# Kernel optimization log

Measured on AMD Instinct MI355X. Metric: run time of the kernel, lower is better.

## Reference

```python
import jax, jax.numpy as jnp
import numpy as np

KSIZE = 3  # module init kwarg


def setup_inputs() -> dict:
    key = jax.random.key(0)
    k1, k2, k3 = jax.random.split(key, 3)
    shape = (16, 3, 512, 512)  # [B, C, H, W]
    return {
        "sr": jax.random.normal(k1, shape, jnp.float32),
        "sr_ema": jax.random.normal(k2, shape, jnp.float32),
        "hr": jax.random.normal(k3, shape, jnp.float32),
    }


def _local_var(res, ksize):
    """Unbiased variance over a ksize x ksize sliding window with reflect pad.

    Matches torch: reflect-pad then unfold + var(unbiased=True). Implemented as a
    box-filter over sum and sum-of-squares (no ksize^2-larger unfold tensor).
    res: [B, 1, H, W] -> [B, 1, H, W]
    """
    pad = (ksize - 1) // 2
    rp = jnp.pad(res, ((0, 0), (0, 0), (pad, pad), (pad, pad)), mode="reflect")
    n = ksize * ksize
    win = (1, 1, ksize, ksize)
    strides = (1, 1, 1, 1)
    zero = jnp.zeros((), rp.dtype)
    s = jax.lax.reduce_window(rp, zero, jax.lax.add, win, strides, "VALID")
    sq = jax.lax.reduce_window(rp * rp, zero, jax.lax.add, win, strides, "VALID")
    # unbiased: (sum(x^2) - sum(x)^2/n) / (n-1)
    return (sq - s * s / n) / (n - 1)


def reference(sr, sr_ema, hr):
    # per-pixel channel-summed residuals, [B, 1, H, W]
    residual_ema = jnp.sum(jnp.abs(hr - sr_ema), axis=1, keepdims=True) / 255.0
    residual_sr = jnp.sum(jnp.abs(hr - sr), axis=1, keepdims=True) / 255.0

    r_det = jax.lax.stop_gradient(residual_sr)  # .clone().detach() in torch

    # patch-level weight: unbiased var over (C=1, H, W) per sample, ** (1/5)
    n_patch = r_det.shape[1] * r_det.shape[2] * r_det.shape[3]
    mean = jnp.mean(r_det, axis=(-1, -2, -3), keepdims=True)
    patch_var = jnp.sum((r_det - mean) ** 2, axis=(-1, -2, -3), keepdims=True) / (n_patch - 1)
    patch_w = patch_var ** 0.2  # [B,1,1,1]

    pixel_w = _local_var(r_det, KSIZE)  # [B,1,H,W]

    overall_w = patch_w * pixel_w
    overall_w = jnp.where(residual_sr < residual_ema, jnp.zeros((), overall_w.dtype), overall_w)

    # L1 loss (mean reduction) between weighted sr and weighted hr
    return jnp.mean(jnp.abs(overall_w * sr - overall_w * hr))
```

## Files before the change

kernel.cpp:

```cpp
#include <hip/hip_runtime.h>
#include <math.h>


#define BB 16
#define HH 512
#define WW 512
#define HW (HH * WW)
#define CHW (3 * HW)
#define STRIPS 128
#define NBLOCKS (BB * STRIPS)
#define NREGIONS NBLOCKS
#define REG_PER_B STRIPS

__device__ __forceinline__ int reflect_h(int gh) {
  gh = gh < 0 ? -gh : gh;
  return gh >= HH ? 2 * HH - 2 - gh : gh;
}

__global__ __launch_bounds__(256, 8) void wl1_main(
    const float* __restrict__ sr, const float* __restrict__ srema,
    const float* __restrict__ hr, float* __restrict__ p_sum,
    float* __restrict__ p_sum2, float* __restrict__ p_loss) {
  __shared__ float rt[6][WW];
  __shared__ float ft[4][WW];
  const int tid = threadIdx.x;
  const int bid = blockIdx.x;
  const int b = bid >> 7;
  const int h0 = (bid & 127) << 2;
  const float* __restrict__ srb = sr + (size_t)b * CHW;
  const float* __restrict__ hrb = hr + (size_t)b * CHW;
  const float* __restrict__ emb = srema + (size_t)b * CHW;

#pragma unroll
  for (int it = 0; it < 3; ++it) {
    const int item = it * 256 + tid;
    const int row = item >> 7;
    const int g = item & 127;
    const int gh = reflect_h(h0 - 1 + row);
    const float* hp = hrb + gh * WW + 4 * g;
    const float* sp = srb + gh * WW + 4 * g;
    float4 h0v = *(const float4*)hp;
    float4 h1v = *(const float4*)(hp + HW);
    float4 h2v = *(const float4*)(hp + 2 * HW);
    float4 s0v = *(const float4*)sp;
    float4 s1v = *(const float4*)(sp + HW);
    float4 s2v = *(const float4*)(sp + 2 * HW);
    float4 r4;
    r4.x = (fabsf(h0v.x - s0v.x) + fabsf(h1v.x - s1v.x) + fabsf(h2v.x - s2v.x)) / 255.0f;
    r4.y = (fabsf(h0v.y - s0v.y) + fabsf(h1v.y - s1v.y) + fabsf(h2v.y - s2v.y)) / 255.0f;
    r4.z = (fabsf(h0v.z - s0v.z) + fabsf(h1v.z - s1v.z) + fabsf(h2v.z - s2v.z)) / 255.0f;
    r4.w = (fabsf(h0v.w - s0v.w) + fabsf(h1v.w - s1v.w) + fabsf(h2v.w - s2v.w)) / 255.0f;
    *(float4*)&rt[row][4 * g] = r4;
    if (row >= 1 && row <= 4) {
      const float* ep = emb + gh * WW + 4 * g;
      float4 e0v = *(const float4*)ep;
      float4 e1v = *(const float4*)(ep + HW);
      float4 e2v = *(const float4*)(ep + 2 * HW);
      float4 e4, f4;
      e4.x = (fabsf(h0v.x - e0v.x) + fabsf(h1v.x - e1v.x) + fabsf(h2v.x - e2v.x)) / 255.0f;
      e4.y = (fabsf(h0v.y - e0v.y) + fabsf(h1v.y - e1v.y) + fabsf(h2v.y - e2v.y)) / 255.0f;
      e4.z = (fabsf(h0v.z - e0v.z) + fabsf(h1v.z - e1v.z) + fabsf(h2v.z - e2v.z)) / 255.0f;
      e4.w = (fabsf(h0v.w - e0v.w) + fabsf(h1v.w - e1v.w) + fabsf(h2v.w - e2v.w)) / 255.0f;
      f4.x = (r4.x >= e4.x) ? 255.0f * r4.x : 0.0f;
      f4.y = (r4.y >= e4.y) ? 255.0f * r4.y : 0.0f;
      f4.z = (r4.z >= e4.z) ? 255.0f * r4.z : 0.0f;
      f4.w = (r4.w >= e4.w) ? 255.0f * r4.w : 0.0f;
      *(float4*)&ft[row - 1][4 * g] = f4;
    }
  }
  __syncthreads();

  const int g = tid & 127;
  const int r0 = tid >> 7;
  const int li = (g == 0) ? 1 : 4 * g - 1;
  const int ri = (g == 127) ? 510 : 4 * g + 4;
  float v1 = 0.f, v2 = 0.f, v3 = 0.f;
#pragma unroll
  for (int k = 0; k < 2; ++k) {
    const int orow = r0 + 2 * k;
    float cs[6] = {0, 0, 0, 0, 0, 0}, cq[6] = {0, 0, 0, 0, 0, 0};
    float center[4];
#pragma unroll
    for (int dr = 0; dr < 3; ++dr) {
      const int row = orow + dr;
      float4 c4 = *(const float4*)&rt[row][4 * g];
      float lv = rt[row][li];
      float rv = rt[row][ri];
      float v[6] = {lv, c4.x, c4.y, c4.z, c4.w, rv};
#pragma unroll
      for (int j = 0; j < 6; ++j) {
        cs[j] += v[j];
        cq[j] += v[j] * v[j];
      }
      if (dr == 1) { center[0] = c4.x; center[1] = c4.y; center[2] = c4.z; center[3] = c4.w; }
    }
    float4 f4 = *(const float4*)&ft[orow][4 * g];
    const float fv[4] = {f4.x, f4.y, f4.z, f4.w};
#pragma unroll
    for (int c = 0; c < 4; ++c) {
      float s = cs[c] + cs[c + 1] + cs[c + 2];
      float q = cq[c] + cq[c + 1] + cq[c + 2];
      float pvar = (q - s * s / 9.0f) / 8.0f;
      float rc = center[c];
      v1 += rc;
      v2 += rc * rc;
      v3 += pvar * fv[c];
    }
  }

#pragma unroll
  for (int off = 32; off > 0; off >>= 1) {
    v1 += __shfl_down(v1, off, 64);
    v2 += __shfl_down(v2, off, 64);
    v3 += __shfl_down(v3, off, 64);
  }
  __syncthreads();
  const int wave = tid >> 6, lane = tid & 63;
  if (lane == 0) {
    rt[0][wave] = v1;
    rt[0][8 + wave] = v2;
    rt[0][16 + wave] = v3;
  }
  __syncthreads();
  if (tid == 0) {
    p_sum[bid] = rt[0][0] + rt[0][1] + rt[0][2] + rt[0][3];
    p_sum2[bid] = rt[0][8] + rt[0][9] + rt[0][10] + rt[0][11];
    p_loss[bid] = rt[0][16] + rt[0][17] + rt[0][18] + rt[0][19];
  }
}

__global__ __launch_bounds__(1024) void wl1_reduce(
    const float* __restrict__ p_sum, const float* __restrict__ p_sum2,
    const float* __restrict__ p_loss, float* __restrict__ out) {
  const int tid = threadIdx.x;
  const int b = tid >> 6, k = tid & 63;
  double s = 0.0, s2 = 0.0, sl = 0.0;
#pragma unroll
  for (int j = 0; j < REG_PER_B; j += 64) {
    int i = b * REG_PER_B + j + k;
    s += (double)p_sum[i];
    s2 += (double)p_sum2[i];
    sl += (double)p_loss[i];
  }
#pragma unroll
  for (int off = 32; off > 0; off >>= 1) {
    s += __shfl_down(s, off, 64);
    s2 += __shfl_down(s2, off, 64);
    sl += __shfl_down(sl, off, 64);
  }
  __shared__ double acc[BB];
  if (k == 0) {
    const double n = (double)HW;
    double var = (s2 - s * s / n) / (n - 1.0);
    acc[b] = pow(var, 0.2) * sl;
  }
  __syncthreads();
  if (tid == 0) {
    double tot = 0.0;
#pragma unroll
    for (int j = 0; j < BB; ++j) tot += acc[j];
    out[0] = (float)(tot / (double)((size_t)BB * CHW));
  }
}

extern "C" void kernel_launch(void* const* d_in, const int* in_sizes, int n_in,
                              void* d_out, int out_size, void* d_ws,
                              size_t ws_size, hipStream_t stream) {
  const float* sr = (const float*)d_in[0];
  const float* srema = (const float*)d_in[1];
  const float* hr = (const float*)d_in[2];
  float* out = (float*)d_out;

  float* p_sum = (float*)d_ws;
  float* p_sum2 = p_sum + NREGIONS;
  float* p_loss = p_sum2 + NREGIONS;

  wl1_main<<<NBLOCKS, 256, 0, stream>>>(sr, srema, hr, p_sum, p_sum2, p_loss);
  wl1_reduce<<<1, 1024, 0, stream>>>(p_sum, p_sum2, p_loss, out);
}
```

Baseline: 163.7 us.

## Split into streaming residual pass and halo-based local-variance pass

The fused kernel is split in two. A streaming first pass reads sr, sr_ema and hr exactly once. It computes the per-pixel residual, folds the ema mask into the sign bit of a compact float4 buffer, and produces per-block sum and sum-of-squares. A second pass reads only that small residual buffer, including halo rows, to compute the 3x3 local variance and the masked loss. This removes the halo re-reads of the large 3-channel inputs, at the cost of an extra kernel launch and a write plus re-read of an intermediate buffer.

```diff
diff --git a/kernel.cpp b/kernel.cpp
--- a/kernel.cpp
+++ b/kernel.cpp
@@ -7,29 +7,81 @@
 #define WW 512
 #define HW (HH * WW)
 #define CHW (3 * HW)
+#define GRP_PER_B (HW / 4)
+#define NGRP (BB * GRP_PER_B)
+#define P1_BLOCKS (NGRP / 256)
+#define P1_PER_B 256
 #define STRIPS 128
-#define NBLOCKS (BB * STRIPS)
-#define NREGIONS NBLOCKS
-#define REG_PER_B STRIPS
+#define P2_BLOCKS (BB * STRIPS)
+#define P2_PER_B STRIPS
 
 __device__ __forceinline__ int reflect_h(int gh) {
   gh = gh < 0 ? -gh : gh;
   return gh >= HH ? 2 * HH - 2 - gh : gh;
 }
 
-__global__ __launch_bounds__(256, 8) void wl1_main(
+__global__ __launch_bounds__(256) void wl1_pass1(
     const float* __restrict__ sr, const float* __restrict__ srema,
-    const float* __restrict__ hr, float* __restrict__ p_sum,
-    float* __restrict__ p_sum2, float* __restrict__ p_loss) {
+    const float* __restrict__ hr, float4* __restrict__ rfbuf,
+    float* __restrict__ p_sum, float* __restrict__ p_sum2) {
+  const int tid = threadIdx.x;
+  const int g = blockIdx.x * 256 + tid;
+  const int b = g >> 16;
+  const int pix = g & 65535;
+  const float* __restrict__ sp = sr + (size_t)b * CHW + 4 * pix;
+  const float* __restrict__ hp = hr + (size_t)b * CHW + 4 * pix;
+  const float* __restrict__ mp = srema + (size_t)b * CHW + 4 * pix;
+
+  float4 s0 = *(const float4*)sp;
+  float4 s1 = *(const float4*)(sp + HW);
+  float4 s2 = *(const float4*)(sp + 2 * HW);
+  float4 h0 = *(const float4*)hp;
+  float4 h1 = *(const float4*)(hp + HW);
+  float4 h2 = *(const float4*)(hp + 2 * HW);
+  float4 m0 = *(const float4*)mp;
+  float4 m1 = *(const float4*)(mp + HW);
+  float4 m2 = *(const float4*)(mp + 2 * HW);
+
+  float4 r4, e4, o4;
+  r4.x = (fabsf(h0.x - s0.x) + fabsf(h1.x - s1.x) + fabsf(h2.x - s2.x)) / 255.0f;
+  r4.y = (fabsf(h0.y - s0.y) + fabsf(h1.y - s1.y) + fabsf(h2.y - s2.y)) / 255.0f;
+  r4.z = (fabsf(h0.z - s0.z) + fabsf(h1.z - s1.z) + fabsf(h2.z - s2.z)) / 255.0f;
+  r4.w = (fabsf(h0.w - s0.w) + fabsf(h1.w - s1.w) + fabsf(h2.w - s2.w)) / 255.0f;
+  e4.x = (fabsf(h0.x - m0.x) + fabsf(h1.x - m1.x) + fabsf(h2.x - m2.x)) / 255.0f;
+  e4.y = (fabsf(h0.y - m0.y) + fabsf(h1.y - m1.y) + fabsf(h2.y - m2.y)) / 255.0f;
+  e4.z = (fabsf(h0.z - m0.z) + fabsf(h1.z - m1.z) + fabsf(h2.z - m2.z)) / 255.0f;
+  e4.w = (fabsf(h0.w - m0.w) + fabsf(h1.w - m1.w) + fabsf(h2.w - m2.w)) / 255.0f;
+  o4.x = (r4.x < e4.x) ? -r4.x : r4.x;
+  o4.y = (r4.y < e4.y) ? -r4.y : r4.y;
+  o4.z = (r4.z < e4.z) ? -r4.z : r4.z;
+  o4.w = (r4.w < e4.w) ? -r4.w : r4.w;
+  rfbuf[g] = o4;
+
+  float v1 = r4.x + r4.y + r4.z + r4.w;
+  float v2 = r4.x * r4.x + r4.y * r4.y + r4.z * r4.z + r4.w * r4.w;
+#pragma unroll
+  for (int off = 32; off > 0; off >>= 1) {
+    v1 += __shfl_down(v1, off, 64);
+    v2 += __shfl_down(v2, off, 64);
+  }
+  __shared__ float red[2][4];
+  const int wave = tid >> 6, lane = tid & 63;
+  if (lane == 0) { red[0][wave] = v1; red[1][wave] = v2; }
+  __syncthreads();
+  if (tid == 0) {
+    p_sum[blockIdx.x] = red[0][0] + red[0][1] + red[0][2] + red[0][3];
+    p_sum2[blockIdx.x] = red[1][0] + red[1][1] + red[1][2] + red[1][3];
+  }
+}
+
+__global__ __launch_bounds__(256, 8) void wl1_pass2(
+    const float4* __restrict__ rfbuf, float* __restrict__ p_loss) {
   __shared__ float rt[6][WW];
   __shared__ float ft[4][WW];
   const int tid = threadIdx.x;
   const int bid = blockIdx.x;
   const int b = bid >> 7;
   const int h0 = (bid & 127) << 2;
-  const float* __restrict__ srb = sr + (size_t)b * CHW;
-  const float* __restrict__ hrb = hr + (size_t)b * CHW;
-  const float* __restrict__ emb = srema + (size_t)b * CHW;
 
 #pragma unroll
   for (int it = 0; it < 3; ++it) {
@@ -37,34 +89,16 @@
     const int row = item >> 7;
     const int g = item & 127;
     const int gh = reflect_h(h0 - 1 + row);
-    const float* hp = hrb + gh * WW + 4 * g;
-    const float* sp = srb + gh * WW + 4 * g;
-    float4 h0v = *(const float4*)hp;
-    float4 h1v = *(const float4*)(hp + HW);
-    float4 h2v = *(const float4*)(hp + 2 * HW);
-    float4 s0v = *(const float4*)sp;
-    float4 s1v = *(const float4*)(sp + HW);
-    float4 s2v = *(const float4*)(sp + 2 * HW);
-    float4 r4;
-    r4.x = (fabsf(h0v.x - s0v.x) + fabsf(h1v.x - s1v.x) + fabsf(h2v.x - s2v.x)) / 255.0f;
-    r4.y = (fabsf(h0v.y - s0v.y) + fabsf(h1v.y - s1v.y) + fabsf(h2v.y - s2v.y)) / 255.0f;
-    r4.z = (fabsf(h0v.z - s0v.z) + fabsf(h1v.z - s1v.z) + fabsf(h2v.z - s2v.z)) / 255.0f;
-    r4.w = (fabsf(h0v.w - s0v.w) + fabsf(h1v.w - s1v.w) + fabsf(h2v.w - s2v.w)) / 255.0f;
-    *(float4*)&rt[row][4 * g] = r4;
+    float4 v = rfbuf[(b << 16) + gh * 128 + g];
+    float4 a4;
+    a4.x = fabsf(v.x); a4.y = fabsf(v.y); a4.z = fabsf(v.z); a4.w = fabsf(v.w);
+    *(float4*)&rt[row][4 * g] = a4;
     if (row >= 1 && row <= 4) {
-      const float* ep = emb + gh * WW + 4 * g;
-      float4 e0v = *(const float4*)ep;
-      float4 e1v = *(const float4*)(ep + HW);
-      float4 e2v = *(const float4*)(ep + 2 * HW);
-      float4 e4, f4;
-      e4.x = (fabsf(h0v.x - e0v.x) + fabsf(h1v.x - e1v.x) + fabsf(h2v.x - e2v.x)) / 255.0f;
-      e4.y = (fabsf(h0v.y - e0v.y) + fabsf(h1v.y - e1v.y) + fabsf(h2v.y - e2v.y)) / 255.0f;
-      e4.z = (fabsf(h0v.z - e0v.z) + fabsf(h1v.z - e1v.z) + fabsf(h2v.z - e2v.z)) / 255.0f;
-      e4.w = (fabsf(h0v.w - e0v.w) + fabsf(h1v.w - e1v.w) + fabsf(h2v.w - e2v.w)) / 255.0f;
-      f4.x = (r4.x >= e4.x) ? 255.0f * r4.x : 0.0f;
-      f4.y = (r4.y >= e4.y) ? 255.0f * r4.y : 0.0f;
-      f4.z = (r4.z >= e4.z) ? 255.0f * r4.z : 0.0f;
-      f4.w = (r4.w >= e4.w) ? 255.0f * r4.w : 0.0f;
+      float4 f4;
+      f4.x = (__float_as_uint(v.x) >> 31) ? 0.0f : 255.0f * a4.x;
+      f4.y = (__float_as_uint(v.y) >> 31) ? 0.0f : 255.0f * a4.y;
+      f4.z = (__float_as_uint(v.z) >> 31) ? 0.0f : 255.0f * a4.z;
+      f4.w = (__float_as_uint(v.w) >> 31) ? 0.0f : 255.0f * a4.w;
       *(float4*)&ft[row - 1][4 * g] = f4;
     }
   }
@@ -74,12 +108,11 @@
   const int r0 = tid >> 7;
   const int li = (g == 0) ? 1 : 4 * g - 1;
   const int ri = (g == 127) ? 510 : 4 * g + 4;
-  float v1 = 0.f, v2 = 0.f, v3 = 0.f;
+  float v3 = 0.f;
 #pragma unroll
   for (int k = 0; k < 2; ++k) {
     const int orow = r0 + 2 * k;
     float cs[6] = {0, 0, 0, 0, 0, 0}, cq[6] = {0, 0, 0, 0, 0, 0};
-    float center[4];
 #pragma unroll
     for (int dr = 0; dr < 3; ++dr) {
       const int row = orow + dr;
@@ -92,7 +125,6 @@
         cs[j] += v[j];
         cq[j] += v[j] * v[j];
       }
-      if (dr == 1) { center[0] = c4.x; center[1] = c4.y; center[2] = c4.z; center[3] = c4.w; }
     }
     float4 f4 = *(const float4*)&ft[orow][4 * g];
     const float fv[4] = {f4.x, f4.y, f4.z, f4.w};
@@ -101,32 +133,17 @@
       float s = cs[c] + cs[c + 1] + cs[c + 2];
       float q = cq[c] + cq[c + 1] + cq[c + 2];
       float pvar = (q - s * s / 9.0f) / 8.0f;
-      float rc = center[c];
-      v1 += rc;
-      v2 += rc * rc;
       v3 += pvar * fv[c];
     }
   }
 
 #pragma unroll
-  for (int off = 32; off > 0; off >>= 1) {
-    v1 += __shfl_down(v1, off, 64);
-    v2 += __shfl_down(v2, off, 64);
-    v3 += __shfl_down(v3, off, 64);
-  }
+  for (int off = 32; off > 0; off >>= 1) v3 += __shfl_down(v3, off, 64);
   __syncthreads();
   const int wave = tid >> 6, lane = tid & 63;
-  if (lane == 0) {
-    rt[0][wave] = v1;
-    rt[0][8 + wave] = v2;
-    rt[0][16 + wave] = v3;
-  }
-  __syncthreads();
-  if (tid == 0) {
-    p_sum[bid] = rt[0][0] + rt[0][1] + rt[0][2] + rt[0][3];
-    p_sum2[bid] = rt[0][8] + rt[0][9] + rt[0][10] + rt[0][11];
-    p_loss[bid] = rt[0][16] + rt[0][17] + rt[0][18] + rt[0][19];
-  }
+  if (lane == 0) rt[0][wave] = v3;
+  __syncthreads();
+  if (tid == 0) p_loss[bid] = rt[0][0] + rt[0][1] + rt[0][2] + rt[0][3];
 }
 
 __global__ __launch_bounds__(1024) void wl1_reduce(
@@ -136,11 +153,14 @@
   const int b = tid >> 6, k = tid & 63;
   double s = 0.0, s2 = 0.0, sl = 0.0;
 #pragma unroll
-  for (int j = 0; j < REG_PER_B; j += 64) {
-    int i = b * REG_PER_B + j + k;
+  for (int j = 0; j < P1_PER_B; j += 64) {
+    int i = b * P1_PER_B + j + k;
     s += (double)p_sum[i];
     s2 += (double)p_sum2[i];
-    sl += (double)p_loss[i];
+  }
+#pragma unroll
+  for (int j = 0; j < P2_PER_B; j += 64) {
+    sl += (double)p_loss[b * P2_PER_B + j + k];
   }
 #pragma unroll
   for (int off = 32; off > 0; off >>= 1) {
@@ -171,10 +191,12 @@
   const float* hr = (const float*)d_in[2];
   float* out = (float*)d_out;
 
-  float* p_sum = (float*)d_ws;
-  float* p_sum2 = p_sum + NREGIONS;
-  float* p_loss = p_sum2 + NREGIONS;
-
-  wl1_main<<<NBLOCKS, 256, 0, stream>>>(sr, srema, hr, p_sum, p_sum2, p_loss);
+  float4* rfbuf = (float4*)d_ws;
+  float* p_sum = (float*)((char*)d_ws + (size_t)NGRP * sizeof(float4));
+  float* p_sum2 = p_sum + P1_BLOCKS;
+  float* p_loss = p_sum2 + P1_BLOCKS;
+
+  wl1_pass1<<<P1_BLOCKS, 256, 0, stream>>>(sr, srema, hr, rfbuf, p_sum, p_sum2);
+  wl1_pass2<<<P2_BLOCKS, 256, 0, stream>>>(rfbuf, p_loss);
   wl1_reduce<<<1, 1024, 0, stream>>>(p_sum, p_sum2, p_loss, out);
 }
```

Measured after the change: 172.4 us. 1.05x slower.
